# Kernel tuning notes

Hardware: AMD Instinct MI355X
Metric: run time of the kernel (lower is better)

## Reference

```python
import jax, jax.numpy as jnp
import numpy as np

B, P, N, E = 4, 8, 4096, 65536
CIN, COUT = 64, 64


def setup_inputs() -> dict:
    key = jax.random.key(0)
    k1, k2, k3 = jax.random.split(key, 3)
    x = jax.random.normal(k1, (B, P, N, CIN), dtype=jnp.float32)
    edge_index = jax.random.randint(k2, (B, 2, E), 0, N, dtype=jnp.int32)
    # GCNConv linear weight (Glorot-ish) and bias
    W = jax.random.normal(k3, (CIN, COUT), dtype=jnp.float32) * (1.0 / np.sqrt(CIN))
    b = jnp.zeros((COUT,), dtype=jnp.float32)
    prelu_a = jnp.full((1,), 0.25, dtype=jnp.float32)  # nn.PReLU default init
    return {"x": x, "edge_index": edge_index, "W": W, "b": b, "prelu_a": prelu_a}


def _gcn_one_graph(x_b, ei, W, b):
    # x_b: [P, N, Cin]; ei: [2, E]. GCNConv with self-loops + symmetric norm,
    # applied to all P frames at once (batched over the frame axis).
    loops = jnp.arange(N, dtype=ei.dtype)
    src = jnp.concatenate([ei[0], loops])  # [E+N] source nodes j
    dst = jnp.concatenate([ei[1], loops])  # [E+N] target nodes i
    deg = jax.ops.segment_sum(jnp.ones(E + N, dtype=x_b.dtype), dst, num_segments=N)
    dinv = jnp.where(deg > 0, jax.lax.rsqrt(deg), jnp.zeros_like(deg))
    norm = dinv[src] * dinv[dst]  # [E+N]
    h = jnp.einsum('pnc,cd->npd', x_b, W)  # [N, P, Cout] (edge axis must lead the gather)
    msgs = norm[:, None, None] * h[src]  # [E+N, P, Cout]
    agg = jax.ops.segment_sum(msgs, dst, num_segments=N)  # [N, P, Cout]
    return jnp.transpose(agg, (1, 0, 2)) + b  # [P, N, Cout]


def reference(x, edge_index, W, b, prelu_a):
    # Fused/batched equivalent of the per-(b,p) Python loop in the torch module.
    out = jax.vmap(_gcn_one_graph, in_axes=(0, 0, None, None))(x, edge_index, W, b)
    # PReLU with single shared slope
    return jnp.where(out >= 0, out, prelu_a * out)
```

## Files before the change

kernel.cpp:

```cpp
#include <hip/hip_runtime.h>

#define BB 4
#define PP 8
#define NN 4096
#define EE 65536
#define SLOTS 48

#define OFF_DEG    33554432u
#define OFF_BUCKET 33619968u

__global__ __launch_bounds__(256) void k_fused(const float* __restrict__ x,
                                               const float* __restrict__ W,
                                               float* __restrict__ h,
                                               const int* __restrict__ ei,
                                               int* __restrict__ deg,
                                               int* __restrict__ bucket) {
    if (blockIdx.x < 2048) {
        __shared__ __align__(16) float xl[64 * 64];
        const int lane = threadIdx.x & 63;
        const int wv   = threadIdx.x >> 6;

        float wreg[64];
#pragma unroll
        for (int k = 0; k < 64; ++k) wreg[k] = W[k * 64 + lane];

        const size_t base = (size_t)blockIdx.x * 64 * 64;
        const float4* xg = (const float4*)(x + base);
        float4* xs = (float4*)xl;
#pragma unroll
        for (int j = 0; j < 4; ++j)
            xs[j * 256 + threadIdx.x] = xg[j * 256 + threadIdx.x];
        __syncthreads();

        float* hb = h + base;
#pragma unroll 1
        for (int r0 = wv * 16; r0 < wv * 16 + 16; r0 += 2) {
            const float4* xa = (const float4*)&xl[r0 * 64];
            const float4* xb = (const float4*)&xl[(r0 + 1) * 64];
            float a0 = 0.f, a1 = 0.f, b0 = 0.f, b1 = 0.f;
#pragma unroll
            for (int k4 = 0; k4 < 16; k4 += 2) {
                const float4 va0 = xa[k4], va1 = xa[k4 + 1];
                const float4 vb0 = xb[k4], vb1 = xb[k4 + 1];
                a0 = fmaf(va0.x, wreg[4 * k4 + 0], a0);
                a0 = fmaf(va0.y, wreg[4 * k4 + 1], a0);
                a0 = fmaf(va0.z, wreg[4 * k4 + 2], a0);
                a0 = fmaf(va0.w, wreg[4 * k4 + 3], a0);
                a1 = fmaf(va1.x, wreg[4 * k4 + 4], a1);
                a1 = fmaf(va1.y, wreg[4 * k4 + 5], a1);
                a1 = fmaf(va1.z, wreg[4 * k4 + 6], a1);
                a1 = fmaf(va1.w, wreg[4 * k4 + 7], a1);
                b0 = fmaf(vb0.x, wreg[4 * k4 + 0], b0);
                b0 = fmaf(vb0.y, wreg[4 * k4 + 1], b0);
                b0 = fmaf(vb0.z, wreg[4 * k4 + 2], b0);
                b0 = fmaf(vb0.w, wreg[4 * k4 + 3], b0);
                b1 = fmaf(vb1.x, wreg[4 * k4 + 4], b1);
                b1 = fmaf(vb1.y, wreg[4 * k4 + 5], b1);
                b1 = fmaf(vb1.z, wreg[4 * k4 + 6], b1);
                b1 = fmaf(vb1.w, wreg[4 * k4 + 7], b1);
            }
            hb[r0 * 64 + lane] = a0 + a1;
            hb[(r0 + 1) * 64 + lane] = b0 + b1;
        }
    } else {
        const int idx = (blockIdx.x - 2048) * 256 + threadIdx.x;
        const int b = idx >> 16;
        const int e = idx & (EE - 1);
        const int s = ei[(size_t)b * 2 * EE + e];
        const int d = ei[(size_t)b * 2 * EE + EE + e];
        const int pos = atomicAdd(&deg[b * NN + d], 1);
        if (pos < SLOTS)
            bucket[(size_t)(b * NN + d) * SLOTS + pos] = s;
    }
}

__global__ __launch_bounds__(256) void k_agg(const float* __restrict__ h,
                                             const int* __restrict__ deg,
                                             const int* __restrict__ bucket,
                                             const float* __restrict__ bias,
                                             const float* __restrict__ pa,
                                             float* __restrict__ out) {
    const int lane = threadIdx.x & 63;
    const int wv   = threadIdx.x >> 6;
    const int g    = blockIdx.x;
    const int q    = g & 7;
    const int idx  = g >> 3;
    const int b    = q >> 1;
    const int i    = (idx << 2) + wv;

    const int* dgb = deg + b * NN;
    const int  ndr = dgb[i];
    const int  nd  = min(ndr, SLOTS);
    const float di = rsqrtf((float)(ndr + 1));
    const int* bk  = bucket + (size_t)(b * NN + i) * SLOTS;
    const float* h0 = h + ((size_t)(q * 4 + 0) << 18);
    const float* h1 = h + ((size_t)(q * 4 + 1) << 18);
    const float* h2 = h + ((size_t)(q * 4 + 2) << 18);
    const float* h3 = h + ((size_t)(q * 4 + 3) << 18);

    const int self = (i << 6) + lane;
    float a0 = di * h0[self];
    float a1 = di * h1[self];
    float a2 = di * h2[self];
    float a3 = di * h3[self];
    float c0 = 0.f, c1 = 0.f, c2 = 0.f, c3 = 0.f;

    int e = 0;
    for (; e + 2 <= nd; e += 2) {
        const int2 jj = *(const int2*)(bk + e);
        const int o0 = (jj.x << 6) + lane;
        const int o1 = (jj.y << 6) + lane;
        const float w0 = rsqrtf((float)(dgb[jj.x] + 1));
        const float w1 = rsqrtf((float)(dgb[jj.y] + 1));
        a0 = fmaf(w0, h0[o0], a0);
        a1 = fmaf(w0, h1[o0], a1);
        a2 = fmaf(w0, h2[o0], a2);
        a3 = fmaf(w0, h3[o0], a3);
        c0 = fmaf(w1, h0[o1], c0);
        c1 = fmaf(w1, h1[o1], c1);
        c2 = fmaf(w1, h2[o1], c2);
        c3 = fmaf(w1, h3[o1], c3);
    }
    if (e < nd) {
        const int j = bk[e];
        const int o = (j << 6) + lane;
        const float w = rsqrtf((float)(dgb[j] + 1));
        a0 = fmaf(w, h0[o], a0);
        a1 = fmaf(w, h1[o], a1);
        a2 = fmaf(w, h2[o], a2);
        a3 = fmaf(w, h3[o], a3);
    }
    a0 += c0; a1 += c1; a2 += c2; a3 += c3;

    const float bs = bias[lane];
    const float al = pa[0];
    float r0 = fmaf(di, a0, bs);
    float r1 = fmaf(di, a1, bs);
    float r2 = fmaf(di, a2, bs);
    float r3 = fmaf(di, a3, bs);
    r0 = r0 >= 0.f ? r0 : al * r0;
    r1 = r1 >= 0.f ? r1 : al * r1;
    r2 = r2 >= 0.f ? r2 : al * r2;
    r3 = r3 >= 0.f ? r3 : al * r3;
    out[((size_t)(q * 4 + 0) << 18) + self] = r0;
    out[((size_t)(q * 4 + 1) << 18) + self] = r1;
    out[((size_t)(q * 4 + 2) << 18) + self] = r2;
    out[((size_t)(q * 4 + 3) << 18) + self] = r3;
}

extern "C" void kernel_launch(void* const* d_in, const int* in_sizes, int n_in,
                              void* d_out, int out_size, void* d_ws, size_t ws_size,
                              hipStream_t stream) {
    const float* x    = (const float*)d_in[0];
    const int*   ei   = (const int*)d_in[1];
    const float* W    = (const float*)d_in[2];
    const float* bias = (const float*)d_in[3];
    const float* pa   = (const float*)d_in[4];
    float* out = (float*)d_out;

    char* ws = (char*)d_ws;
    float* h      = (float*)ws;
    int*   deg    = (int*)(ws + OFF_DEG);
    int*   bucket = (int*)(ws + OFF_BUCKET);

    hipMemsetAsync(deg, 0, BB * NN * sizeof(int), stream);

    k_fused<<<3072, 256, 0, stream>>>(x, W, h, ei, deg, bucket);
    k_agg<<<(BB * PP * NN) / 16, 256, 0, stream>>>(h, deg, bucket, bias, pa, out);
}
```

Before: 151.3 us.

## Remap block indices so each XCD owns contiguous frames for L2 locality

The transform blocks are remapped so that blocks dispatched round-robin to the same XCD (blockIdx & 7) process the frames that the same XCD will later aggregate. The aggregation kernel now handles two frames per block instead of four, doubles the grid, and unrolls neighbor gathers by four with independent accumulators. The aim is for each XCD's private L2 to hold only its own slice of h, which cuts cross-XCD misses during the random gather. The costs are more redundant index and degree loads per frame and a reliance on the hardware's round-robin XCD dispatch.

```diff
diff --git a/kernel.cpp b/kernel.cpp
--- a/kernel.cpp
+++ b/kernel.cpp
@@ -24,7 +24,13 @@
 #pragma unroll
         for (int k = 0; k < 64; ++k) wreg[k] = W[k * 64 + lane];
 
-        const size_t base = (size_t)blockIdx.x * 64 * 64;
+        const int bid = blockIdx.x;
+        const int xcd = bid & 7;
+        const int kk  = bid >> 3;
+        const int f   = xcd * 4 + (kk >> 6);
+        const int rb  = kk & 63;
+        const size_t base = ((size_t)f * NN + rb * 64) * 64;
+
         const float4* xg = (const float4*)(x + base);
         float4* xs = (float4*)xl;
 #pragma unroll
@@ -83,69 +89,63 @@
     const int lane = threadIdx.x & 63;
     const int wv   = threadIdx.x >> 6;
     const int g    = blockIdx.x;
-    const int q    = g & 7;
+    const int xcd  = g & 7;
     const int idx  = g >> 3;
-    const int b    = q >> 1;
-    const int i    = (idx << 2) + wv;
+    const int pair = xcd * 2 + (idx >> 10);
+    const int bp0  = pair * 2;
+    const int b    = bp0 >> 3;
+    const int i    = ((idx & 1023) << 2) + wv;
 
     const int* dgb = deg + b * NN;
     const int  ndr = dgb[i];
     const int  nd  = min(ndr, SLOTS);
     const float di = rsqrtf((float)(ndr + 1));
     const int* bk  = bucket + (size_t)(b * NN + i) * SLOTS;
-    const float* h0 = h + ((size_t)(q * 4 + 0) << 18);
-    const float* h1 = h + ((size_t)(q * 4 + 1) << 18);
-    const float* h2 = h + ((size_t)(q * 4 + 2) << 18);
-    const float* h3 = h + ((size_t)(q * 4 + 3) << 18);
+    const float* h0 = h + ((size_t)bp0 << 18);
+    const float* h1 = h0 + (1u << 18);
 
     const int self = (i << 6) + lane;
-    float a0 = di * h0[self];
-    float a1 = di * h1[self];
-    float a2 = di * h2[self];
-    float a3 = di * h3[self];
-    float c0 = 0.f, c1 = 0.f, c2 = 0.f, c3 = 0.f;
+    float a00 = di * h0[self], a01 = 0.f, a02 = 0.f, a03 = 0.f;
+    float a10 = di * h1[self], a11 = 0.f, a12 = 0.f, a13 = 0.f;
 
     int e = 0;
-    for (; e + 2 <= nd; e += 2) {
-        const int2 jj = *(const int2*)(bk + e);
+    for (; e + 4 <= nd; e += 4) {
+        const int4 jj = *(const int4*)(bk + e);
+        const float w0 = rsqrtf((float)(dgb[jj.x] + 1));
+        const float w1 = rsqrtf((float)(dgb[jj.y] + 1));
+        const float w2 = rsqrtf((float)(dgb[jj.z] + 1));
+        const float w3 = rsqrtf((float)(dgb[jj.w] + 1));
         const int o0 = (jj.x << 6) + lane;
         const int o1 = (jj.y << 6) + lane;
-        const float w0 = rsqrtf((float)(dgb[jj.x] + 1));
-        const float w1 = rsqrtf((float)(dgb[jj.y] + 1));
-        a0 = fmaf(w0, h0[o0], a0);
-        a1 = fmaf(w0, h1[o0], a1);
-        a2 = fmaf(w0, h2[o0], a2);
-        a3 = fmaf(w0, h3[o0], a3);
-        c0 = fmaf(w1, h0[o1], c0);
-        c1 = fmaf(w1, h1[o1], c1);
-        c2 = fmaf(w1, h2[o1], c2);
-        c3 = fmaf(w1, h3[o1], c3);
+        const int o2 = (jj.z << 6) + lane;
+        const int o3 = (jj.w << 6) + lane;
+        a00 = fmaf(w0, h0[o0], a00);
+        a10 = fmaf(w0, h1[o0], a10);
+        a01 = fmaf(w1, h0[o1], a01);
+        a11 = fmaf(w1, h1[o1], a11);
+        a02 = fmaf(w2, h0[o2], a02);
+        a12 = fmaf(w2, h1[o2], a12);
+        a03 = fmaf(w3, h0[o3], a03);
+        a13 = fmaf(w3, h1[o3], a13);
     }
-    if (e < nd) {
+    for (; e < nd; ++e) {
         const int j = bk[e];
         const int o = (j << 6) + lane;
         const float w = rsqrtf((float)(dgb[j] + 1));
-        a0 = fmaf(w, h0[o], a0);
-        a1 = fmaf(w, h1[o], a1);
-        a2 = fmaf(w, h2[o], a2);
-        a3 = fmaf(w, h3[o], a3);
+        a00 = fmaf(w, h0[o], a00);
+        a10 = fmaf(w, h1[o], a10);
     }
-    a0 += c0; a1 += c1; a2 += c2; a3 += c3;
+    const float acc0 = (a00 + a01) + (a02 + a03);
+    const float acc1 = (a10 + a11) + (a12 + a13);
 
     const float bs = bias[lane];
     const float al = pa[0];
-    float r0 = fmaf(di, a0, bs);
-    float r1 = fmaf(di, a1, bs);
-    float r2 = fmaf(di, a2, bs);
-    float r3 = fmaf(di, a3, bs);
+    float r0 = fmaf(di, acc0, bs);
+    float r1 = fmaf(di, acc1, bs);
     r0 = r0 >= 0.f ? r0 : al * r0;
     r1 = r1 >= 0.f ? r1 : al * r1;
-    r2 = r2 >= 0.f ? r2 : al * r2;
-    r3 = r3 >= 0.f ? r3 : al * r3;
-    out[((size_t)(q * 4 + 0) << 18) + self] = r0;
-    out[((size_t)(q * 4 + 1) << 18) + self] = r1;
-    out[((size_t)(q * 4 + 2) << 18) + self] = r2;
-    out[((size_t)(q * 4 + 3) << 18) + self] = r3;
+    out[((size_t)bp0 << 18) + self] = r0;
+    out[(((size_t)bp0 + 1) << 18) + self] = r1;
 }
 
 extern "C" void kernel_launch(void* const* d_in, const int* in_sizes, int n_in,
@@ -166,5 +166,5 @@
     hipMemsetAsync(deg, 0, BB * NN * sizeof(int), stream);
 
     k_fused<<<3072, 256, 0, stream>>>(x, W, h, ei, deg, bucket);
-    k_agg<<<(BB * PP * NN) / 16, 256, 0, stream>>>(h, deg, bucket, bias, pa, out);
+    k_agg<<<(BB * PP * NN) / 8, 256, 0, stream>>>(h, deg, bucket, bias, pa, out);
 }
```

New measurement: 157.4 us. +4.1%, slower.
